# Performance work log

Hardware: AMD Instinct MI355X
Metric: run time of the kernel (lower is better)

Reference implementation:

```python
import jax, jax.numpy as jnp
import numpy as np

N_NODES = 100000
N_EDGES = 3200000
D_IN = 128
D_OUT = 128


def setup_inputs() -> dict:
    key = jax.random.key(0)
    k1, k2, k3, k4, k5 = jax.random.split(key, 5)
    x = jax.random.normal(k1, (N_NODES, D_IN), dtype=jnp.float32)
    adj_rows = jax.random.randint(k2, (N_EDGES,), 0, N_NODES, dtype=jnp.int64)
    adj_cols = jax.random.randint(k3, (N_EDGES,), 0, N_NODES, dtype=jnp.int64)
    adj_vals = jax.random.uniform(k4, (N_EDGES,), dtype=jnp.float32)
    # torch Linear weight has shape (dim_out, dim_in)
    W = jax.random.normal(k5, (D_OUT, D_IN), dtype=jnp.float32) * (1.0 / np.sqrt(D_IN))
    return {"x": x, "adj_rows": adj_rows, "adj_cols": adj_cols, "adj_vals": adj_vals, "W": W}


def reference(x, adj_rows, adj_cols, adj_vals, W):
    # h = Linear(x) with no bias: x @ W^T  -> [N, D_OUT]
    h = x @ W.T
    # sparse.mm(adjacency, h): out[r] = sum_e vals[e] * h[cols[e]] for edges with rows[e]==r
    msgs = adj_vals[:, None] * h[adj_cols]           # [E, D_OUT]
    agg = jax.ops.segment_sum(msgs, adj_rows, num_segments=N_NODES)
    return jax.nn.relu(agg)
```

## Files before the change

### kernel.cpp

```cpp
#include <hip/hip_runtime.h>
#include <stdint.h>

typedef unsigned short u16;
typedef unsigned int u32;
typedef __attribute__((ext_vector_type(8))) short short8;
typedef __attribute__((ext_vector_type(4))) float floatx4;

#define DIM 128
#define DIM2 64
#define NBK 2048
#define NB_SH 6
#define AGG_NB 64
#define AGG_C 1024
#define SC_C 4096

__device__ __forceinline__ u32 f32_to_bf16_rne(float f) {
  u32 u = __float_as_uint(f);
  u32 r = u + 0x7fffu + ((u >> 16) & 1u);
  return r >> 16;
}
__device__ __forceinline__ float bf16_to_f32(u32 u) { return __uint_as_float(u << 16); }
__device__ __forceinline__ u32 pack2bf16(float a, float b) {
  return f32_to_bf16_rne(a) | (f32_to_bf16_rne(b) << 16);
}

union FragU {
  u32 d[4];
  short8 s;
};

__global__ __launch_bounds__(256) void gemm_mfma(const float* __restrict__ x,
                                                 const float* __restrict__ W,
                                                 u16* __restrict__ h, int N) {
  __shared__ u32 Wl[DIM * DIM2];
  int tid = threadIdx.x;
#pragma unroll
  for (int i = 0; i < 8; ++i) {
    int ga = tid + 256 * i;
    int o = ga >> 4, g = ga & 15;
    const float* src = W + (size_t)o * DIM + g * 8;
    floatx4 f0 = *(const floatx4*)src;
    floatx4 f1 = *(const floatx4*)(src + 4);
    int slot = (g + o) & 15;
    u32* dst = &Wl[o * DIM2 + slot * 4];
    dst[0] = pack2bf16(f0.x, f0.y);
    dst[1] = pack2bf16(f0.z, f0.w);
    dst[2] = pack2bf16(f1.x, f1.y);
    dst[3] = pack2bf16(f1.z, f1.w);
  }
  __syncthreads();

  int lane = tid & 63;
  int wave = tid >> 6;
  int nodeBase = (blockIdx.x * 4 + wave) * 16;
  if (nodeBase >= N) return;
  int m = lane & 15;
  int kg = lane >> 4;

  short8 a[4];
  const float* xr = x + (size_t)(nodeBase + m) * DIM + kg * 8;
#pragma unroll
  for (int kt = 0; kt < 4; ++kt) {
    floatx4 f0 = *(const floatx4*)(xr + kt * 32);
    floatx4 f1 = *(const floatx4*)(xr + kt * 32 + 4);
    FragU fu;
    fu.d[0] = pack2bf16(f0.x, f0.y);
    fu.d[1] = pack2bf16(f0.z, f0.w);
    fu.d[2] = pack2bf16(f1.x, f1.y);
    fu.d[3] = pack2bf16(f1.z, f1.w);
    a[kt] = fu.s;
  }

#pragma unroll
  for (int ot = 0; ot < 8; ++ot) {
    int o = ot * 16 + m;
    floatx4 acc = {0.f, 0.f, 0.f, 0.f};
#pragma unroll
    for (int kt = 0; kt < 4; ++kt) {
      int slot = (kt * 4 + kg + o) & 15;
      short8 b = *(short8*)&Wl[o * DIM2 + slot * 4];
      acc = __builtin_amdgcn_mfma_f32_16x16x32_bf16(a[kt], b, acc, 0, 0, 0);
    }
#pragma unroll
    for (int r = 0; r < 4; ++r) {
      int node = nodeBase + kg * 4 + r;
      h[(size_t)node * DIM + ot * 16 + m] = (u16)f32_to_bf16_rne(acc[r]);
    }
  }
}

__global__ void zero_kernel(int* __restrict__ p, int n) {
  int i = blockIdx.x * blockDim.x + threadIdx.x;
  if (i < n) p[i] = 0;
}

__device__ __forceinline__ void scan2048(u32* cnt, u32* excl, u32* wtot) {
  int tid = threadIdx.x, lane = tid & 63, wave = tid >> 6;
  u32 c[8], sum = 0;
#pragma unroll
  for (int k = 0; k < 8; ++k) {
    c[k] = cnt[tid * 8 + k];
    sum += c[k];
  }
  u32 inc = sum;
#pragma unroll
  for (int d = 1; d < 64; d <<= 1) {
    u32 t = __shfl_up(inc, d, 64);
    if (lane >= d) inc += t;
  }
  if (lane == 63) wtot[wave] = inc;
  __syncthreads();
  u32 wbase = 0;
  for (int w = 0; w < wave; ++w) wbase += wtot[w];
  u32 run = wbase + inc - sum;
#pragma unroll
  for (int k = 0; k < 8; ++k) {
    excl[tid * 8 + k] = run;
    run += c[k];
  }
  __syncthreads();
}

__global__ __launch_bounds__(256) void bucket_hist(const int* __restrict__ rows,
                                                   int* __restrict__ bhist, int E, int B) {
  __shared__ u32 hist[NBK];
  int tid = threadIdx.x;
  for (int b = tid; b < NBK; b += 256) hist[b] = 0;
  __syncthreads();
  int base = blockIdx.x * SC_C;
  for (int j = tid; j < SC_C; j += 256) {
    int e = base + j;
    if (e < E) atomicAdd(&hist[((u32)rows[e]) >> NB_SH], 1u);
  }
  __syncthreads();
  for (int b = tid; b < B; b += 256) {
    u32 c = hist[b];
    if (c) atomicAdd(&bhist[b], (int)c);
  }
}

__global__ __launch_bounds__(256) void bucket_scan(const int* __restrict__ bhist,
                                                   int* __restrict__ bbase,
                                                   int* __restrict__ bptr) {
  __shared__ u32 cnt[NBK], excl[NBK], wtot[4];
  int tid = threadIdx.x;
  for (int b = tid; b < NBK; b += 256) cnt[b] = (u32)bhist[b];
  __syncthreads();
  scan2048(cnt, excl, wtot);
  for (int b = tid; b < NBK; b += 256) {
    bbase[b] = (int)excl[b];
    bptr[b] = (int)excl[b];
  }
}

__global__ __launch_bounds__(256) void bin_scatter(const int* __restrict__ rows,
                                                   const int* __restrict__ cols,
                                                   const float* __restrict__ vals,
                                                   int* __restrict__ bptr,
                                                   u32* __restrict__ bcol,
                                                   u16* __restrict__ bval, int E) {
  __shared__ u32 hist[NBK], starts[NBK], roff[NBK], gbase[NBK], wtot[4];
  __shared__ u32 s_col[SC_C];
  __shared__ u16 s_val[SC_C];
  __shared__ u16 s_bkt[SC_C];
  int tid = threadIdx.x;
  int base = blockIdx.x * SC_C;
  int tot = min(SC_C, E - base);

  for (int b = tid; b < NBK; b += 256) hist[b] = 0;
  __syncthreads();
  for (int j = tid; j < tot; j += 256) {
    atomicAdd(&hist[((u32)rows[base + j]) >> NB_SH], 1u);
  }
  __syncthreads();
  scan2048(hist, starts, wtot);
  for (int b = tid; b < NBK; b += 256) {
    u32 c = hist[b];
    roff[b] = starts[b];
    gbase[b] = c ? (u32)atomicAdd(&bptr[b], (int)c) : 0u;
  }
  __syncthreads();
  for (int j = tid; j < tot; j += 256) {
    int e = base + j;
    u32 r = (u32)rows[e];
    u32 b = r >> NB_SH;
    u32 p = atomicAdd(&roff[b], 1u);
    s_col[p] = (u32)cols[e] | ((r & ((1u << NB_SH) - 1u)) << 17);
    s_val[p] = (u16)f32_to_bf16_rne(vals[e]);
    s_bkt[p] = (u16)b;
  }
  __syncthreads();
  for (int i = tid; i < tot; i += 256) {
    u32 b = s_bkt[i];
    u32 d = gbase[b] + ((u32)i - starts[b]);
    bcol[d] = s_col[i];
    bval[d] = s_val[i];
  }
}

__global__ __launch_bounds__(256) void agg_bucket(const int* __restrict__ bhist,
                                                  const int* __restrict__ bbase,
                                                  const u32* __restrict__ bcol,
                                                  const u16* __restrict__ bval,
                                                  const u32* __restrict__ h,
                                                  float* __restrict__ out, int N) {
  __shared__ floatx4 accv[AGG_NB * DIM / 4];
  __shared__ u32 s_col[AGG_C];
  __shared__ u16 s_val[AGG_C];
  __shared__ u32 cnt[AGG_NB], excl[AGG_NB], ptr[AGG_NB];
  float* acc = (float*)accv;
  int tid = threadIdx.x, lane = tid & 63, wave = tid >> 6;
  int b = blockIdx.x;
  floatx4 zv = {0.f, 0.f, 0.f, 0.f};
  for (int i = tid; i < AGG_NB * DIM / 4; i += 256) accv[i] = zv;

  int base = bbase[b], T = bhist[b];

  float a0 = 0.f, a1 = 0.f;
  int curn = -1;

  for (int c0 = 0; c0 < T; c0 += AGG_C) {
    int n = min(AGG_C, T - c0);
    if (tid < AGG_NB) cnt[tid] = 0;
    __syncthreads();
    u32 rc[4], rb[4];
#pragma unroll
    for (int k = 0; k < 4; ++k) {
      rc[k] = 0;
      rb[k] = 0;
      int j = tid + 256 * k;
      if (j < n) {
        rc[k] = bcol[base + c0 + j];
        rb[k] = bval[base + c0 + j];
        atomicAdd(&cnt[rc[k] >> 17], 1u);
      }
    }
    __syncthreads();
    if (tid < 64) {
      u32 c = cnt[tid];
      u32 inc = c;
#pragma unroll
      for (int d = 1; d < 64; d <<= 1) {
        u32 t = __shfl_up(inc, d, 64);
        if (lane >= d) inc += t;
      }
      excl[tid] = inc - c;
      ptr[tid] = inc - c;
    }
    __syncthreads();
#pragma unroll
    for (int k = 0; k < 4; ++k) {
      int j = tid + 256 * k;
      if (j < n) {
        u32 p = atomicAdd(&ptr[rc[k] >> 17], 1u);
        s_col[p] = rc[k];
        s_val[p] = (u16)rb[k];
      }
    }
    __syncthreads();
    int wbeg = (int)excl[wave * 16];
    int wend = (int)ptr[wave * 16 + 15];
    for (int e = wbeg; e < wend; e += 16) {
      u32 mt[16];
      float vv[16];
#pragma unroll
      for (int g = 0; g < 16; ++g) {
        int ee = e + g;
        bool act = ee < wend;
        int idx = act ? ee : (wend - 1);
        mt[g] = s_col[idx];
        vv[g] = act ? bf16_to_f32(s_val[idx]) : 0.f;
      }
      u32 hd[16];
#pragma unroll
      for (int g = 0; g < 16; ++g) {
        hd[g] = h[(size_t)(mt[g] & 0x1FFFFu) * DIM2 + lane];
      }
#pragma unroll
      for (int g = 0; g < 16; ++g) {
        int nid = __builtin_amdgcn_readfirstlane((int)(mt[g] >> 17));
        if (nid != curn) {
          if (curn >= 0) {
            float2* ap = (float2*)&acc[curn * DIM + 2 * lane];
            float2 t = *ap;
            t.x += a0;
            t.y += a1;
            *ap = t;
          }
          curn = nid;
          a0 = 0.f;
          a1 = 0.f;
        }
        float v = vv[g];
        a0 += v * bf16_to_f32(hd[g] & 0xffffu);
        a1 += v * bf16_to_f32(hd[g] >> 16);
      }
    }
  }
  if (curn >= 0) {
    float2* ap = (float2*)&acc[curn * DIM + 2 * lane];
    float2 t = *ap;
    t.x += a0;
    t.y += a1;
    *ap = t;
  }
  __syncthreads();

  int nodeBase = b * AGG_NB;
  for (int i = tid; i < AGG_NB * DIM / 4; i += 256) {
    int r = i >> 5;
    int node = nodeBase + r;
    if (node < N) {
      floatx4 a = accv[i];
      floatx4 o = {fmaxf(a.x, 0.f), fmaxf(a.y, 0.f), fmaxf(a.z, 0.f), fmaxf(a.w, 0.f)};
      *(floatx4*)(out + (size_t)node * DIM + (i & 31) * 4) = o;
    }
  }
}

extern "C" void kernel_launch(void* const* d_in, const int* in_sizes, int n_in,
                              void* d_out, int out_size, void* d_ws, size_t ws_size,
                              hipStream_t stream) {
  const float* x    = (const float*)d_in[0];
  const int*   rows = (const int*)d_in[1];
  const int*   cols = (const int*)d_in[2];
  const float* vals = (const float*)d_in[3];
  const float* W    = (const float*)d_in[4];

  const int N = in_sizes[0] / DIM;
  const int E = in_sizes[1];
  const int B = (N + AGG_NB - 1) / AGG_NB;

  char* wsb = (char*)d_ws;
  size_t o = 0;
  u16* h = (u16*)wsb;                    o += (size_t)N * DIM * sizeof(u16);
  int* bhist = (int*)(wsb + o);          o += (size_t)NBK * 4;
  int* bbase = (int*)(wsb + o);          o += (size_t)NBK * 4;
  int* bptr  = (int*)(wsb + o);          o += (size_t)NBK * 4;
  u32* bcol  = (u32*)(wsb + o);          o += (size_t)E * 4;
  u16* bval  = (u16*)(wsb + o);          o += (size_t)E * 2;

  const int nsc = (E + SC_C - 1) / SC_C;

  zero_kernel<<<(NBK + 255) / 256, 256, 0, stream>>>(bhist, NBK);
  gemm_mfma<<<(N + 63) / 64, 256, 0, stream>>>(x, W, h, N);
  bucket_hist<<<nsc, 256, 0, stream>>>(rows, bhist, E, B);
  bucket_scan<<<1, 256, 0, stream>>>(bhist, bbase, bptr);
  bin_scatter<<<nsc, 256, 0, stream>>>(rows, cols, vals, bptr, bcol, bval, E);
  agg_bucket<<<B, 256, 0, stream>>>(bhist, bbase, bcol, bval, (const u32*)h,
                                    (float*)d_out, N);
}
```

Baseline: 400.0 us.

## Single-pass bucket aggregation with packed 64-bit records and direct output writes

The aggregation kernel now loads the whole bucket (up to 2560 edges) in one pass instead of chunks of 1024. Each edge's column byte-offset, local row and value are packed into one 64-bit shared-memory record. Because a bucket's edges are fully sorted by local node, each wave writes its node results with ReLU straight to global memory, which removes the shared 64x128 float accumulator, its zeroing and the final copy. Empty nodes get explicit zero writes. A slow fallback loop handles buckets larger than the cap, and the gather inner loop shrinks from 16 to 8 edges, which may reduce memory-level parallelism.

Result: faster. 361.9 us (-9.5%).

```diff
diff --git a/kernel.cpp b/kernel.cpp
--- a/kernel.cpp
+++ b/kernel.cpp
@@ -3,6 +3,7 @@
 
 typedef unsigned short u16;
 typedef unsigned int u32;
+typedef unsigned long long u64;
 typedef __attribute__((ext_vector_type(8))) short short8;
 typedef __attribute__((ext_vector_type(4))) float floatx4;
 
@@ -11,7 +12,7 @@
 #define NBK 2048
 #define NB_SH 6
 #define AGG_NB 64
-#define AGG_C 1024
+#define AGG_CAP 2560
 #define SC_C 4096
 
 __device__ __forceinline__ u32 f32_to_bf16_rne(float f) {
@@ -159,8 +160,11 @@
                                                    int* __restrict__ bptr,
                                                    u32* __restrict__ bcol,
                                                    u16* __restrict__ bval, int E) {
-  __shared__ u32 hist[NBK], starts[NBK], roff[NBK], gbase[NBK], wtot[4];
-  __shared__ u32 s_col[SC_C];
+  __shared__ u32 hist[NBK];
+  __shared__ u32 starts[NBK];
+  __shared__ u32 gbase[NBK];
+  __shared__ u32 wtot[4];
+  __shared__ u32 s_lo[SC_C];
   __shared__ u16 s_val[SC_C];
   __shared__ u16 s_bkt[SC_C];
   int tid = threadIdx.x;
@@ -176,24 +180,24 @@
   scan2048(hist, starts, wtot);
   for (int b = tid; b < NBK; b += 256) {
     u32 c = hist[b];
-    roff[b] = starts[b];
     gbase[b] = c ? (u32)atomicAdd(&bptr[b], (int)c) : 0u;
+    hist[b] = starts[b];
   }
   __syncthreads();
   for (int j = tid; j < tot; j += 256) {
     int e = base + j;
     u32 r = (u32)rows[e];
-    u32 b = r >> NB_SH;
-    u32 p = atomicAdd(&roff[b], 1u);
-    s_col[p] = (u32)cols[e] | ((r & ((1u << NB_SH) - 1u)) << 17);
+    u32 bk = r >> NB_SH;
+    u32 p = atomicAdd(&hist[bk], 1u);
+    s_lo[p] = ((r & 63u) << 26) | ((u32)cols[e] << 8);
     s_val[p] = (u16)f32_to_bf16_rne(vals[e]);
-    s_bkt[p] = (u16)b;
+    s_bkt[p] = (u16)bk;
   }
   __syncthreads();
   for (int i = tid; i < tot; i += 256) {
-    u32 b = s_bkt[i];
-    u32 d = gbase[b] + ((u32)i - starts[b]);
-    bcol[d] = s_col[i];
+    u32 bk = s_bkt[i];
+    u32 d = gbase[bk] + ((u32)i - starts[bk]);
+    bcol[d] = s_lo[i];
     bval[d] = s_val[i];
   }
 }
@@ -204,41 +208,33 @@
                                                   const u16* __restrict__ bval,
                                                   const u32* __restrict__ h,
                                                   float* __restrict__ out, int N) {
-  __shared__ floatx4 accv[AGG_NB * DIM / 4];
-  __shared__ u32 s_col[AGG_C];
-  __shared__ u16 s_val[AGG_C];
+  __shared__ u64 s_rec[AGG_CAP];
   __shared__ u32 cnt[AGG_NB], excl[AGG_NB], ptr[AGG_NB];
-  float* acc = (float*)accv;
   int tid = threadIdx.x, lane = tid & 63, wave = tid >> 6;
   int b = blockIdx.x;
-  floatx4 zv = {0.f, 0.f, 0.f, 0.f};
-  for (int i = tid; i < AGG_NB * DIM / 4; i += 256) accv[i] = zv;
-
   int base = bbase[b], T = bhist[b];
-
-  float a0 = 0.f, a1 = 0.f;
-  int curn = -1;
-
-  for (int c0 = 0; c0 < T; c0 += AGG_C) {
-    int n = min(AGG_C, T - c0);
+  int nodeBase = b << NB_SH;
+  int lane4 = lane * 4;
+  const char* hb = (const char*)h;
+
+  if (T <= AGG_CAP) {
     if (tid < AGG_NB) cnt[tid] = 0;
     __syncthreads();
-    u32 rc[4], rb[4];
-#pragma unroll
-    for (int k = 0; k < 4; ++k) {
-      rc[k] = 0;
-      rb[k] = 0;
+    u32 rlo[10], rv[10];
+#pragma unroll
+    for (int k = 0; k < 10; ++k) {
       int j = tid + 256 * k;
-      if (j < n) {
-        rc[k] = bcol[base + c0 + j];
-        rb[k] = bval[base + c0 + j];
-        atomicAdd(&cnt[rc[k] >> 17], 1u);
+      rlo[k] = 0;
+      rv[k] = 0;
+      if (j < T) {
+        rlo[k] = bcol[base + j];
+        rv[k] = bval[base + j];
+        atomicAdd(&cnt[rlo[k] >> 26], 1u);
       }
     }
     __syncthreads();
     if (tid < 64) {
-      u32 c = cnt[tid];
-      u32 inc = c;
+      u32 c = cnt[tid], inc = c;
 #pragma unroll
       for (int d = 1; d < 64; d <<= 1) {
         u32 t = __shfl_up(inc, d, 64);
@@ -249,71 +245,79 @@
     }
     __syncthreads();
 #pragma unroll
-    for (int k = 0; k < 4; ++k) {
+    for (int k = 0; k < 10; ++k) {
       int j = tid + 256 * k;
-      if (j < n) {
-        u32 p = atomicAdd(&ptr[rc[k] >> 17], 1u);
-        s_col[p] = rc[k];
-        s_val[p] = (u16)rb[k];
+      if (j < T) {
+        u32 p = atomicAdd(&ptr[rlo[k] >> 26], 1u);
+        s_rec[p] = ((u64)(rv[k] << 16) << 32) | rlo[k];
       }
     }
     __syncthreads();
     int wbeg = (int)excl[wave * 16];
     int wend = (int)ptr[wave * 16 + 15];
-    for (int e = wbeg; e < wend; e += 16) {
-      u32 mt[16];
-      float vv[16];
-#pragma unroll
-      for (int g = 0; g < 16; ++g) {
+    float a0 = 0.f, a1 = 0.f;
+    int curn = -1;
+    for (int e = wbeg; e < wend; e += 8) {
+      u32 lo8[8];
+      float v8[8];
+      u32 hd[8];
+#pragma unroll
+      for (int g = 0; g < 8; ++g) {
         int ee = e + g;
         bool act = ee < wend;
-        int idx = act ? ee : (wend - 1);
-        mt[g] = s_col[idx];
-        vv[g] = act ? bf16_to_f32(s_val[idx]) : 0.f;
-      }
-      u32 hd[16];
-#pragma unroll
-      for (int g = 0; g < 16; ++g) {
-        hd[g] = h[(size_t)(mt[g] & 0x1FFFFu) * DIM2 + lane];
-      }
-#pragma unroll
-      for (int g = 0; g < 16; ++g) {
-        int nid = __builtin_amdgcn_readfirstlane((int)(mt[g] >> 17));
+        u64 r = s_rec[act ? ee : (wend - 1)];
+        lo8[g] = (u32)r;
+        v8[g] = act ? __uint_as_float((u32)(r >> 32)) : 0.f;
+      }
+#pragma unroll
+      for (int g = 0; g < 8; ++g) {
+        hd[g] = *(const u32*)(hb + ((lo8[g] & 0x01FFFF00u) + lane4));
+      }
+#pragma unroll
+      for (int g = 0; g < 8; ++g) {
+        int nid = __builtin_amdgcn_readfirstlane((int)(lo8[g] >> 26));
         if (nid != curn) {
           if (curn >= 0) {
-            float2* ap = (float2*)&acc[curn * DIM + 2 * lane];
-            float2 t = *ap;
-            t.x += a0;
-            t.y += a1;
-            *ap = t;
+            float2 o = make_float2(fmaxf(a0, 0.f), fmaxf(a1, 0.f));
+            *(float2*)(out + (size_t)(nodeBase + curn) * DIM + 2 * lane) = o;
           }
           curn = nid;
           a0 = 0.f;
           a1 = 0.f;
         }
-        float v = vv[g];
+        float v = v8[g];
         a0 += v * bf16_to_f32(hd[g] & 0xffffu);
         a1 += v * bf16_to_f32(hd[g] >> 16);
       }
     }
-  }
-  if (curn >= 0) {
-    float2* ap = (float2*)&acc[curn * DIM + 2 * lane];
-    float2 t = *ap;
-    t.x += a0;
-    t.y += a1;
-    *ap = t;
-  }
-  __syncthreads();
-
-  int nodeBase = b * AGG_NB;
-  for (int i = tid; i < AGG_NB * DIM / 4; i += 256) {
-    int r = i >> 5;
-    int node = nodeBase + r;
-    if (node < N) {
-      floatx4 a = accv[i];
-      floatx4 o = {fmaxf(a.x, 0.f), fmaxf(a.y, 0.f), fmaxf(a.z, 0.f), fmaxf(a.w, 0.f)};
-      *(floatx4*)(out + (size_t)node * DIM + (i & 31) * 4) = o;
+    if (curn >= 0) {
+      float2 o = make_float2(fmaxf(a0, 0.f), fmaxf(a1, 0.f));
+      *(float2*)(out + (size_t)(nodeBase + curn) * DIM + 2 * lane) = o;
+    }
+    for (int nn = 0; nn < 16; ++nn) {
+      int nl = wave * 16 + nn;
+      int node = nodeBase + nl;
+      if (cnt[nl] == 0 && node < N) {
+        *(float2*)(out + (size_t)node * DIM + 2 * lane) = make_float2(0.f, 0.f);
+      }
+    }
+  } else {
+    for (int nn = 0; nn < 16; ++nn) {
+      int nl = wave * 16 + nn;
+      int node = nodeBase + nl;
+      if (node >= N) continue;
+      float a0 = 0.f, a1 = 0.f;
+      for (int e = 0; e < T; ++e) {
+        u32 lo = bcol[base + e];
+        if ((int)(lo >> 26) == nl) {
+          u32 d = *(const u32*)(hb + ((lo & 0x01FFFF00u) + lane4));
+          float v = bf16_to_f32(bval[base + e]);
+          a0 += v * bf16_to_f32(d & 0xffffu);
+          a1 += v * bf16_to_f32(d >> 16);
+        }
+      }
+      *(float2*)(out + (size_t)node * DIM + 2 * lane) =
+          make_float2(fmaxf(a0, 0.f), fmaxf(a1, 0.f));
     }
   }
 }
```
